# Performance work log

Hardware: AMD Instinct MI355X
Metric: run time of the kernel (lower is better)

Reference implementation:

```python
import jax, jax.numpy as jnp
import numpy as np

B, T, N, F = 8, 24, 207, 16
H = 64            # hidden_dim
DH = 16           # dims_hyper[-1] / node-embedding out
DA = 4 * F        # temporal attention dim_out
DS = 64           # ss_gal gcn out dim (last_ss_gal_dim)
GDEP = 2
ALPHA, BETA, GAMMA = 0.05, 0.95, 0.95
TA = 2.0


def _lin(x, w, b=None):
    y = x @ w
    return y if b is None else y + b


def gcn_hyper(x, A, W, b):
    # x: [B,N,C], A: [N,N] static. h <- a*x + g * einsum('nvc,vw->nwc', h, A)
    h = x
    outs = [h]
    for _ in range(GDEP):
        h = ALPHA * x + GAMMA * jnp.einsum('bvc,vw->bwc', h, A)
        outs.append(h)
    return _lin(jnp.concatenate(outs, axis=-1), W, b)


def gcn_gru(x, A_dyn, A_sta, W, b):
    # x: [B,N,C], A_dyn: [B,N,N], A_sta: [N,N]
    h = x
    outs = [h]
    for _ in range(GDEP):
        h = (ALPHA * x
             + BETA * jnp.einsum('bvw,bvc->bwc', A_dyn, h)     # bmm(A^T, h)
             + GAMMA * jnp.einsum('bvc,vw->bwc', h, A_sta))
        outs.append(h)
    return _lin(jnp.concatenate(outs, axis=-1), W, b)


def gcn_ssgal(x, A, W, b):
    # x: [B*,N,C], A: [B*,N,N]
    h = x
    outs = [h]
    for _ in range(GDEP):
        h = ALPHA * x + GAMMA * jnp.einsum('bvw,bvc->bwc', A, h)
        outs.append(h)
    return _lin(jnp.concatenate(outs, axis=-1), W, b)


def setup_inputs() -> dict:
    key = jax.random.key(0)
    ks = jax.random.split(key, 32)
    i = iter(range(32))
    w = lambda *s: (0.02 * jax.random.normal(ks[next(i)], s, dtype=jnp.float32))
    inp = {
        'input_sequence': jax.random.normal(ks[next(i)], (B, T, N, F), dtype=jnp.float32),
        'static_adj': jax.random.uniform(ks[next(i)], (N, N), dtype=jnp.float32),
        # hyper graph generators: mlp in = (GDEP+1)*H -> DH
        'src_gen_w': w((GDEP + 1) * H, DH), 'src_gen_b': w(DH),
        'tgt_gen_w': w((GDEP + 1) * H, DH), 'tgt_gen_b': w(DH),
        # node embeddings: F -> DH
        'src_emb_w': w(F, DH), 'src_emb_b': w(DH),
        'tgt_emb_w': w(F, DH), 'tgt_emb_b': w(DH),
        # GRU gate GCNs: mlp in = (GDEP+1)*(F+H) -> H
        'gru_z_w': w((GDEP + 1) * (F + H), H), 'gru_z_b': w(H),
        'gru_r_w': w((GDEP + 1) * (F + H), H), 'gru_r_b': w(H),
        'gru_c_w': w((GDEP + 1) * (F + H), H), 'gru_c_b': w(H),
        # temporal attention: F -> DA, score DA -> 1
        'attn_q_w': w(F, DA),
        'attn_k_w': w(F, DA), 'attn_k_b': w(DA),
        'attn_s_w': w(DA, 1),
        # ss_gal spatial gcn: (GDEP+1)*F -> DS
        'sgcn_w': w((GDEP + 1) * F, DS), 'sgcn_b': w(DS),
        # predictors
        'short_w': w(DS, F), 'short_b': w(F),
        'long_w': w(H, F), 'long_b': w(F),
        'fus_w': w(DS + H, F), 'fus_b': w(F),
    }
    return inp


def _forward(input_sequence, static_adj,
             src_gen_w, src_gen_b, tgt_gen_w, tgt_gen_b,
             src_emb_w, src_emb_b, tgt_emb_w, tgt_emb_b,
             gru_z_w, gru_z_b, gru_r_w, gru_r_b, gru_c_w, gru_c_b,
             attn_q_w, attn_k_w, attn_k_b, attn_s_w,
             sgcn_w, sgcn_b,
             short_w, short_b, long_w, long_b, fus_w, fus_b):
    batch, steps, nodes = input_sequence.shape[0], input_sequence.shape[1], input_sequence.shape[2]
    eye = jnp.eye(nodes, dtype=input_sequence.dtype)

    def cell(x_t, h):
        # x_t: [B,N,F], h: [B,N,H]
        src_ctx = gcn_hyper(h, static_adj, src_gen_w, src_gen_b)   # [B,N,DH]
        tgt_ctx = gcn_hyper(h, static_adj, tgt_gen_w, tgt_gen_b)
        s = jnp.tanh(TA * _lin(x_t, src_emb_w, src_emb_b) * src_ctx)
        t = jnp.tanh(TA * _lin(x_t, tgt_emb_w, tgt_emb_b) * tgt_ctx)
        asym = jnp.einsum('bnc,bmc->bnm', s, t) - jnp.einsum('bnc,bmc->bnm', t, s)
        adj = jax.nn.relu(jnp.tanh(TA * asym)) + eye
        adj = adj / (adj.sum(axis=-1, keepdims=True) + 1e-8)
        gi = jnp.concatenate([x_t, h], axis=-1)
        z = jax.nn.sigmoid(gcn_gru(gi, adj, static_adj, gru_z_w, gru_z_b))
        r = jax.nn.sigmoid(gcn_gru(gi, adj, static_adj, gru_r_w, gru_r_b))
        ri = jnp.concatenate([x_t, r * h], axis=-1)
        c = jnp.tanh(gcn_gru(ri, adj, static_adj, gru_c_w, gru_c_b))
        return z * h + (1.0 - z) * c

    h = jnp.zeros((batch, nodes, H), dtype=input_sequence.dtype)
    for t_step in range(0, max(1, steps - 4), 4):
        h = cell(input_sequence[:, t_step], h)

    # ss_gal branch on the last 4 steps
    recent = input_sequence[:, -4:]            # [B,4,N,F]
    target = input_sequence[:, -1]             # [B,N,F]
    # temporal attention
    q = target @ attn_q_w                      # [B,N,DA]
    k = recent @ attn_k_w + attn_k_b           # [B,4,N,DA]
    scores = jnp.tanh(q[:, None, :, None, :] + k[:, :, None, :, :])  # [B,4,N,N,DA]
    scores = jnp.squeeze(scores @ attn_s_w, axis=-1)                  # [B,4,N,N]
    attn = jax.nn.softmax(scores, axis=-1)
    dyn_adj = static_adj[None] + attn.reshape(-1, nodes, nodes)       # [B*4,N,N]
    rh = recent.reshape(-1, nodes, recent.shape[-1])                  # [B*4,N,F]
    rh = gcn_ssgal(rh, dyn_adj, sgcn_w, sgcn_b)                       # [B*4,N,DS]
    rh = jax.nn.relu(rh.reshape(batch, -1, nodes, rh.shape[-1]))      # [B,4,N,DS]
    target = jnp.sum(rh, axis=1)                                       # [B,N,DS]

    short = _lin(target, short_w, short_b)      # [B,N,F]
    h = cell(short, h)                          # final GRU step on short-term prediction
    long = _lin(h, long_w, long_b)              # [B,N,F]
    fused = _lin(jnp.concatenate([target, h], axis=-1), fus_w, fus_b)  # [B,N,F]
    return jnp.stack([short, long, fused], axis=0)  # [3,B,N,F]


def reference(input_sequence, static_adj,
              src_gen_w, src_gen_b, tgt_gen_w, tgt_gen_b,
              src_emb_w, src_emb_b, tgt_emb_w, tgt_emb_b,
              gru_z_w, gru_z_b, gru_r_w, gru_r_b, gru_c_w, gru_c_b,
              attn_q_w, attn_k_w, attn_k_b, attn_s_w,
              sgcn_w, sgcn_b,
              short_w, short_b, long_w, long_b, fus_w, fus_b):
    return _forward(input_sequence, static_adj,
                    src_gen_w, src_gen_b, tgt_gen_w, tgt_gen_b,
                    src_emb_w, src_emb_b, tgt_emb_w, tgt_emb_b,
                    gru_z_w, gru_z_b, gru_r_w, gru_r_b, gru_c_w, gru_c_b,
                    attn_q_w, attn_k_w, attn_k_b, attn_s_w,
                    sgcn_w, sgcn_b,
                    short_w, short_b, long_w, long_b, fus_w, fus_b)
```

## Files before the change

kernel.cpp:

```cpp
#include <hip/hip_runtime.h>


constexpr int B = 8, T = 24, N = 207, F = 16, H = 64, DH = 16;
constexpr int PS = 208;
constexpr float ALPHA = 0.05f, BETA = 0.95f, GAMMA = 0.95f, TA = 2.0f;
constexpr int NF = N * F;
constexpr int BNF = B * N * F;

__device__ __forceinline__ float tanh_fast(float x) { float e = __expf(2.f * x); return 1.f - 2.f / (e + 1.f); }
__device__ __forceinline__ float sigm(float x) { return 1.f / (1.f + __expf(-x)); }
__device__ __forceinline__ float tanh_poly(float x) {
    float x2 = x * x;
    float c = __builtin_fmaf(x2, 0.13333333f, -0.33333333f);
    return x * __builtin_fmaf(x2, c, 1.f);
}

__global__ __launch_bounds__(256) void k_stage0(
    const float* __restrict__ adj, const float* __restrict__ inp,
    const float* __restrict__ Wq, const float* __restrict__ Wk,
    const float* __restrict__ kb, const float* __restrict__ sw_,
    float* __restrict__ Ts, float* __restrict__ A2,
    float* __restrict__ attnT, float* __restrict__ rsum)
{
    __shared__ __align__(16) float smem[7424];
    int bid = blockIdx.x, tid = threadIdx.x;
    if (bid < 49) {
        int vb = (bid % 7) * 32, wb = (bid / 7) * 32;
        float* sA = smem;
        float* sB = smem + 1056;
        float acc[4] = {0, 0, 0, 0};
        int i0 = tid >> 5, j = tid & 31;
        for (int u0 = 0; u0 < N; u0 += 32) {
            __syncthreads();
            for (int l = tid; l < 1024; l += 256) {
                int i = l >> 5, jj = l & 31;
                int v = vb + i, u = u0 + jj;
                sA[i * 33 + jj] = (v < N && u < N) ? adj[v * N + u] : 0.f;
                int uu = u0 + i, w = wb + jj;
                sB[i * 33 + jj] = (uu < N && w < N) ? adj[uu * N + w] : 0.f;
            }
            __syncthreads();
#pragma unroll 8
            for (int u = 0; u < 32; u++) {
                float bv = sB[u * 33 + j];
#pragma unroll
                for (int k = 0; k < 4; k++) acc[k] += sA[(i0 + k * 8) * 33 + u] * bv;
            }
        }
#pragma unroll
        for (int k = 0; k < 4; k++) {
            int v = vb + i0 + k * 8, w = wb + j;
            if (v < N && w < N) A2[(size_t)w * PS + v] = acc[k];
        }
    } else if (bid < 217) {
        int i = (bid - 49) * 256 + tid;
        if (i < N * N) {
            int w = i / N, v = i % N;
            Ts[(size_t)w * PS + v] = adj[v * N + w];
        }
    } else {
        int idx = bid - 217;
        int bt = idx / 49, rem = idx % 49;
        int n0 = (rem % 7) * 32, m0 = (rem / 7) * 32;
        int b = bt >> 2, tau = bt & 3;
        int ti = tid >> 4, tj = tid & 15;
        float* sQ = smem;
        float* sK = smem + 2080;
        float* sWq = smem + 4160;
        float* sWk = smem + 5184;
        float* sXq = smem + 6208;
        float* sXk = smem + 6752;
        float* ssw = smem + 7296;
        float* skb = smem + 7360;
        const float* xq = inp + ((size_t)(b * T + (T - 1))) * NF;
        const float* xk = inp + ((size_t)(b * T + 20 + tau)) * NF;
        {
            float4 wq4 = *(const float4*)&Wq[tid * 4];
            float4 wk4 = *(const float4*)&Wk[tid * 4];
            *(float4*)&sWq[(tid >> 4) * 64 + (tid & 15) * 4] = wq4;
            *(float4*)&sWk[(tid >> 4) * 64 + (tid & 15) * 4] = wk4;
            if (tid < 64) { ssw[tid] = sw_[tid]; skb[tid] = kb[tid]; }
            int i2 = tid & 127;
            int r = i2 >> 2, c4 = (i2 & 3) * 4;
            if (tid < 128) {
                float4 a = make_float4(0, 0, 0, 0);
                int n = n0 + r;
                if (n < N) a = *(const float4*)&xq[(size_t)n * F + c4];
                sXq[r * 17 + c4] = a.x; sXq[r * 17 + c4 + 1] = a.y; sXq[r * 17 + c4 + 2] = a.z; sXq[r * 17 + c4 + 3] = a.w;
            } else {
                float4 c = make_float4(0, 0, 0, 0);
                int m = m0 + r;
                if (m < N) c = *(const float4*)&xk[(size_t)m * F + c4];
                sXk[r * 17 + c4] = c.x; sXk[r * 17 + c4 + 1] = c.y; sXk[r * 17 + c4 + 2] = c.z; sXk[r * 17 + c4 + 3] = c.w;
            }
        }
        __syncthreads();
        {
            int r = tid >> 3, o0 = (tid & 7) * 8;
            float xr[16], xkr[16];
#pragma unroll
            for (int f = 0; f < 16; f++) { xr[f] = sXq[r * 17 + f]; xkr[f] = sXk[r * 17 + f]; }
#pragma unroll
            for (int j = 0; j < 8; j++) {
                int o = o0 + j;
                float aq = 0.f, ak = skb[o];
#pragma unroll
                for (int f = 0; f < 16; f++) { aq += xr[f] * sWq[f * 64 + o]; ak += xkr[f] * sWk[f * 64 + o]; }
                sQ[r * 65 + o] = aq; sK[r * 65 + o] = ak;
            }
        }
        __syncthreads();
        float s00 = 0.f, s01 = 0.f, s10 = 0.f, s11 = 0.f;
#pragma unroll 2
        for (int d = 0; d < 64; d++) {
            float w = ssw[d];
            float q1 = sQ[ti * 65 + d], q2 = sQ[(ti + 16) * 65 + d];
            float k1 = sK[tj * 65 + d], k2 = sK[(tj + 16) * 65 + d];
            s00 += tanh_poly(q1 + k1) * w;
            s01 += tanh_poly(q1 + k2) * w;
            s10 += tanh_poly(q2 + k1) * w;
            s11 += tanh_poly(q2 + k2) * w;
        }
        int n1 = n0 + ti, n2 = n0 + ti + 16, m1 = m0 + tj, m2 = m0 + tj + 16;
        bool vn1 = n1 < N, vn2 = n2 < N, vm1 = m1 < N, vm2 = m2 < N;
        float e00 = (vn1 && vm1) ? __expf(s00) : 0.f;
        float e01 = (vn1 && vm2) ? __expf(s01) : 0.f;
        float e10 = (vn2 && vm1) ? __expf(s10) : 0.f;
        float e11 = (vn2 && vm2) ? __expf(s11) : 0.f;
        float part1 = e00 + e01, part2 = e10 + e11;
        for (int d = 8; d > 0; d >>= 1) {
            part1 += __shfl_down(part1, d, 16);
            part2 += __shfl_down(part2, d, 16);
        }
        if (tj == 0) {
            if (vn1) atomicAdd(&rsum[bt * N + n1], part1);
            if (vn2) atomicAdd(&rsum[bt * N + n2], part2);
        }
        __syncthreads();
        float* tile = sQ;
        tile[tj * 33 + ti] = e00;
        tile[(tj + 16) * 33 + ti] = e01;
        tile[tj * 33 + ti + 16] = e10;
        tile[(tj + 16) * 33 + ti + 16] = e11;
        __syncthreads();
        {
            int row = tid >> 3, c4 = (tid & 7) * 4;
            int m = m0 + row;
            if (m < N) {
                float4 v = make_float4(tile[row * 33 + c4], tile[row * 33 + c4 + 1],
                                       tile[row * 33 + c4 + 2], tile[row * 33 + c4 + 3]);
                *(float4*)&attnT[(size_t)bt * PS * PS + (size_t)m * PS + n0 + c4] = v;
            }
        }
    }
}

__global__ __launch_bounds__(256) void k_cell_a(
    const float* __restrict__ h, const float* __restrict__ Ts, const float* __restrict__ A2,
    const float* __restrict__ xseq, int tsel, const float* __restrict__ xbuf,
    const float* __restrict__ Wsrc, const float* __restrict__ bsrc,
    const float* __restrict__ Wtgt, const float* __restrict__ btgt,
    const float* __restrict__ Wes, const float* __restrict__ bes,
    const float* __restrict__ Wet, const float* __restrict__ bet,
    float* __restrict__ s_out, float* __restrict__ t_out, float* __restrict__ catg) {
    int b = blockIdx.y, w0 = blockIdx.x * 16, lane = blockIdx.z;
    int tid = threadIdx.x, ty = tid >> 4, tx = tid & 15;
    __shared__ float sTs[2][16][33], sA2[2][16][33];
    __shared__ float sH[2][32][64];
    __shared__ float cat[16][193];
    __shared__ float sW[192][16];
    __shared__ float sX[16][16], sWe[16][16];
    float au[4] = {0, 0, 0, 0}, aw[4] = {0, 0, 0, 0};
    const float* hb = h + b * N * H;
    const float* xp = (tsel >= 0) ? (xseq + ((size_t)(b * T + tsel)) * NF) : (xbuf + (size_t)b * NF);
    int pidx = tid & 127;
    int pr = pidx >> 3, pc4 = (pidx & 7) * 4;
    float4 t4;
    float4 h4[2];
    int hr[2], hc[2];
#pragma unroll
    for (int k = 0; k < 2; k++) { int l4 = tid + k * 256; hr[k] = l4 >> 4; hc[k] = (l4 & 15) * 4; }
    auto loadT = [&](int v0) {
        t4 = make_float4(0, 0, 0, 0);
        const float* src = (tid < 128) ? Ts : A2;
        int w = w0 + pr;
        if (w < N) t4 = *(const float4*)&src[(size_t)w * PS + v0 + pc4];
#pragma unroll
        for (int k = 0; k < 2; k++) {
            float4 hv = make_float4(0, 0, 0, 0);
            int v = v0 + hr[k];
            if (v < N) hv = *(const float4*)&hb[(size_t)v * H + hc[k]];
            h4[k] = hv;
        }
    };
    loadT(0);
    int cur = 0;
    for (int t = 0; t < 7; t++) {
        __syncthreads();
        {
            float (*dst)[33] = (tid < 128) ? sTs[cur] : sA2[cur];
            dst[pr][pc4] = t4.x; dst[pr][pc4 + 1] = t4.y; dst[pr][pc4 + 2] = t4.z; dst[pr][pc4 + 3] = t4.w;
        }
#pragma unroll
        for (int k = 0; k < 2; k++) *(float4*)&sH[cur][hr[k]][hc[k]] = h4[k];
        if (t < 6) loadT((t + 1) * 32);
        __syncthreads();
#pragma unroll 8
        for (int v = 0; v < 32; v++) {
            float pu = sTs[cur][ty][v], pw = sA2[cur][ty][v];
#pragma unroll
            for (int j = 0; j < 4; j++) {
                float x = sH[cur][v][tx * 4 + j];
                au[j] += pu * x; aw[j] += pw * x;
            }
        }
        cur ^= 1;
    }
    int w = w0 + ty;
    bool valid = w < N;
    __syncthreads();
    if (valid) {
#pragma unroll
        for (int j = 0; j < 4; j++) {
            int c = tx * 4 + j;
            float hv = hb[(size_t)w * H + c];
            float u = au[j], w2 = aw[j];
            cat[ty][c] = hv;
            cat[ty][64 + c] = ALPHA * hv + GAMMA * u;
            cat[ty][128 + c] = ALPHA * hv + ALPHA * GAMMA * u + GAMMA * GAMMA * w2;
        }
    } else {
#pragma unroll
        for (int j = 0; j < 4; j++) {
            int c = tx * 4 + j;
            cat[ty][c] = 0; cat[ty][64 + c] = 0; cat[ty][128 + c] = 0;
        }
    }
    const float* Wg = lane ? Wtgt : Wsrc;
    const float* bg = lane ? btgt : bsrc;
    const float* We = lane ? Wet : Wes;
    const float* be = lane ? bet : bes;
    {
        float4 wv[3];
#pragma unroll
        for (int k = 0; k < 3; k++) wv[k] = *(const float4*)&Wg[(tid + k * 256) * 4];
        float4 xv = make_float4(0, 0, 0, 0), ev = make_float4(0, 0, 0, 0);
        int sr = 0, sc = 0;
        if (tid < 64) {
            sr = tid >> 2; sc = (tid & 3) * 4;
            int n = w0 + sr;
            if (n < N) xv = *(const float4*)&xp[(size_t)n * F + sc];
            ev = *(const float4*)&We[tid * 4];
        }
#pragma unroll
        for (int k = 0; k < 3; k++) {
            int l4 = tid + k * 256;
            int r = l4 >> 2, c4 = (l4 & 3) * 4;
            *(float4*)&sW[r][c4] = wv[k];
        }
        if (tid < 64) {
            *(float4*)&sX[sr][sc] = xv;
            *(float4*)&sWe[sr][sc] = ev;
        }
    }
    __syncthreads();
    if (lane == 0 && valid) {
#pragma unroll
        for (int j = 0; j < 5; j++) {
            int c = tx * 5 + j;
            float v = (c < 16) ? sX[ty][c] : hb[(size_t)w * H + (c - 16)];
            catg[((size_t)(b * N + w)) * 80 + c] = v;
        }
    }
    {
        float ctx = bg[tx];
#pragma unroll 8
        for (int c = 0; c < 192; c++) ctx += cat[ty][c] * sW[c][tx];
        float xe = be[tx];
#pragma unroll
        for (int f = 0; f < 16; f++) xe += sX[ty][f] * sWe[f][tx];
        if (valid) {
            float val = tanh_fast(TA * xe * ctx);
            if (lane == 0) s_out[(size_t)(b * N + w) * DH + tx] = val;
            else           t_out[(size_t)(b * N + w) * DH + tx] = val;
        }
    }
}

__global__ __launch_bounds__(256) void k_cell_bP(const float* __restrict__ s_in, const float* __restrict__ t_in,
                                                 const float* __restrict__ adj, float* __restrict__ P) {
    int b = blockIdx.y, v0 = blockIdx.x * 16;
    int tid = threadIdx.x, ty = tid >> 4, tx = tid & 15;
    __shared__ float sS[N][17], sT[N][17];
    for (int l4 = tid; l4 < 828; l4 += 256) {
        float4 sv = *(const float4*)&s_in[(size_t)b * N * 16 + l4 * 4];
        float4 tv = *(const float4*)&t_in[(size_t)b * N * 16 + l4 * 4];
        int r = l4 >> 2, c = (l4 & 3) * 4;
        sS[r][c] = sv.x; sS[r][c + 1] = sv.y; sS[r][c + 2] = sv.z; sS[r][c + 3] = sv.w;
        sT[r][c] = tv.x; sT[r][c + 1] = tv.y; sT[r][c + 2] = tv.z; sT[r][c + 3] = tv.w;
    }
    __syncthreads();
    int v = v0 + ty;
    bool valid = v < N;
    int vc = valid ? v : (N - 1);
    float sv[16], tv[16];
#pragma unroll
    for (int k = 0; k < 16; k++) { sv[k] = sS[vc][k]; tv[k] = sT[vc][k]; }
    float val[13];
    float rsum = 0.f;
#pragma unroll
    for (int idx = 0; idx < 13; idx++) {
        int w = tx + 16 * idx;
        float r = 0.f;
        if (w < N) {
            float a = 0.f;
#pragma unroll
            for (int k = 0; k < 16; k++) a += sv[k] * sT[w][k] - tv[k] * sS[w][k];
            r = tanh_fast(TA * a);
            r = r > 0.f ? r : 0.f;
            if (w == v) r += 1.f;
        }
        val[idx] = r;
        rsum += r;
    }
    float tot = rsum;
    for (int d = 8; d > 0; d >>= 1) tot += __shfl_down(tot, d, 16);
    tot = __shfl(tot, 0, 16);
    float rinv = BETA / (tot + 1e-8f);
    if (valid) {
        float* Pb = P + (size_t)b * PS * PS;
#pragma unroll
        for (int idx = 0; idx < 13; idx++) {
            int w = tx + 16 * idx;
            if (w < N) Pb[(size_t)w * PS + v] = val[idx] * rinv + GAMMA * adj[v * N + w];
        }
    }
}

__device__ __forceinline__ void body_prop_xr(float* smem, int w0, int bt,
    const float* __restrict__ attnT, const float* __restrict__ rsum,
    const float* __restrict__ Ts, const float* __restrict__ inp, float* __restrict__ x1)
{
    int b = bt >> 2, tau = bt & 3;
    const float* xb = inp + ((size_t)(b * T + 20 + tau)) * NF;
    const float* PA = attnT + (size_t)bt * PS * PS;
    int tid = threadIdx.x, ty = tid >> 4, tx = tid & 15;
    float (*sPA)[16][33] = (float(*)[16][33])(smem);
    float (*sPT)[16][33] = (float(*)[16][33])(smem + 1056);
    float (*sX)[32][17]  = (float(*)[32][17])(smem + 2112);
    float (*sXs)[32][17] = (float(*)[32][17])(smem + 3200);
    float accA = 0.f, accT = 0.f;
    int prr = tid >> 3, pcc = (tid & 7) * 4;
    int xrr = (tid - 128) >> 2, xcc = ((tid - 128) & 3) * 4;
    float4 pa, pt, xv;
    float rinv_;
    auto loadT = [&](int v0) {
        pa = make_float4(0, 0, 0, 0); pt = make_float4(0, 0, 0, 0); xv = make_float4(0, 0, 0, 0); rinv_ = 0.f;
        if (tid < 128) {
            int w = w0 + prr;
            if (w < N) {
                pa = *(const float4*)&PA[(size_t)w * PS + v0 + pcc];
                pt = *(const float4*)&Ts[(size_t)w * PS + v0 + pcc];
            }
        } else {
            int v = v0 + xrr;
            if (v < N) {
                xv = *(const float4*)&xb[(size_t)v * F + xcc];
                rinv_ = __builtin_amdgcn_rcpf(rsum[bt * N + v]);
            }
        }
    };
    loadT(0);
    int cur = 0;
    for (int t = 0; t < 7; t++) {
        __syncthreads();
        if (tid < 128) {
            sPA[cur][prr][pcc] = pa.x; sPA[cur][prr][pcc + 1] = pa.y; sPA[cur][prr][pcc + 2] = pa.z; sPA[cur][prr][pcc + 3] = pa.w;
            sPT[cur][prr][pcc] = pt.x; sPT[cur][prr][pcc + 1] = pt.y; sPT[cur][prr][pcc + 2] = pt.z; sPT[cur][prr][pcc + 3] = pt.w;
        } else {
            sX[cur][xrr][xcc] = xv.x; sX[cur][xrr][xcc + 1] = xv.y; sX[cur][xrr][xcc + 2] = xv.z; sX[cur][xrr][xcc + 3] = xv.w;
            sXs[cur][xrr][xcc] = xv.x * rinv_; sXs[cur][xrr][xcc + 1] = xv.y * rinv_;
            sXs[cur][xrr][xcc + 2] = xv.z * rinv_; sXs[cur][xrr][xcc + 3] = xv.w * rinv_;
        }
        if (t < 6) loadT((t + 1) * 32);
        __syncthreads();
#pragma unroll 8
        for (int v = 0; v < 32; v++) {
            accA += sPA[cur][ty][v] * sXs[cur][v][tx];
            accT += sPT[cur][ty][v] * sX[cur][v][tx];
        }
        cur ^= 1;
    }
    int w = w0 + ty;
    if (w < N) x1[((size_t)(bt * N + w)) * 16 + tx] = ALPHA * xb[w * F + tx] + GAMMA * (accA + accT);
}

__device__ __forceinline__ void body_sgc2(float* smem, int w0, int bt,
    const float* __restrict__ attnT, const float* __restrict__ rsum,
    const float* __restrict__ Ts, const float* __restrict__ x1, const float* __restrict__ inp,
    const float* __restrict__ Ws, const float* __restrict__ bs, float* __restrict__ target)
{
    int b = bt >> 2, tau = bt & 3;
    const float* xb = inp + ((size_t)(b * T + 20 + tau)) * NF;
    const float* PA = attnT + (size_t)bt * PS * PS;
    int tid = threadIdx.x, ty = tid >> 4, tx = tid & 15;
    float (*sPA)[16][33] = (float(*)[16][33])(smem);
    float (*sPT)[16][33] = (float(*)[16][33])(smem + 1056);
    float (*sX)[32][17]  = (float(*)[32][17])(smem + 2112);
    float (*sXs)[32][17] = (float(*)[32][17])(smem + 3200);
    float (*scat)[48]    = (float(*)[48])(smem + 4288);
    float (*sWs)[64]     = (float(*)[64])(smem + 5056);
    float accA = 0.f, accT = 0.f;
    int prr = tid >> 3, pcc = (tid & 7) * 4;
    int xrr = (tid - 128) >> 2, xcc = ((tid - 128) & 3) * 4;
    float4 pa, pt, xv;
    float rinv_;
    auto loadT = [&](int v0) {
        pa = make_float4(0, 0, 0, 0); pt = make_float4(0, 0, 0, 0); xv = make_float4(0, 0, 0, 0); rinv_ = 0.f;
        if (tid < 128) {
            int w = w0 + prr;
            if (w < N) {
                pa = *(const float4*)&PA[(size_t)w * PS + v0 + pcc];
                pt = *(const float4*)&Ts[(size_t)w * PS + v0 + pcc];
            }
        } else {
            int v = v0 + xrr;
            if (v < N) {
                xv = *(const float4*)&x1[((size_t)(bt * N + v)) * 16 + xcc];
                rinv_ = __builtin_amdgcn_rcpf(rsum[bt * N + v]);
            }
        }
    };
    loadT(0);
    int cur = 0;
    for (int t = 0; t < 7; t++) {
        __syncthreads();
        if (tid < 128) {
            sPA[cur][prr][pcc] = pa.x; sPA[cur][prr][pcc + 1] = pa.y; sPA[cur][prr][pcc + 2] = pa.z; sPA[cur][prr][pcc + 3] = pa.w;
            sPT[cur][prr][pcc] = pt.x; sPT[cur][prr][pcc + 1] = pt.y; sPT[cur][prr][pcc + 2] = pt.z; sPT[cur][prr][pcc + 3] = pt.w;
        } else {
            sX[cur][xrr][xcc] = xv.x; sX[cur][xrr][xcc + 1] = xv.y; sX[cur][xrr][xcc + 2] = xv.z; sX[cur][xrr][xcc + 3] = xv.w;
            sXs[cur][xrr][xcc] = xv.x * rinv_; sXs[cur][xrr][xcc + 1] = xv.y * rinv_;
            sXs[cur][xrr][xcc + 2] = xv.z * rinv_; sXs[cur][xrr][xcc + 3] = xv.w * rinv_;
        }
        if (t < 6) loadT((t + 1) * 32);
        __syncthreads();
#pragma unroll 8
        for (int v = 0; v < 32; v++) {
            accA += sPA[cur][ty][v] * sXs[cur][v][tx];
            accT += sPT[cur][ty][v] * sX[cur][v][tx];
        }
        cur ^= 1;
    }
    int w = w0 + ty;
    bool valid = w < N;
    __syncthreads();
    for (int l = tid; l < 512; l += 256) {
        int i = l >> 5, c = l & 31;
        int ww = w0 + i;
        float vv = 0;
        if (ww < N) {
            if (c < 16) vv = xb[ww * F + c];
            else vv = x1[((size_t)bt * N + ww) * 16 + (c - 16)];
        }
        scat[i][c] = vv;
    }
    {
        float x0 = valid ? xb[w * F + tx] : 0.f;
        scat[ty][32 + tx] = ALPHA * x0 + GAMMA * (accA + accT);
    }
    {
        float4 wv[3];
#pragma unroll
        for (int k = 0; k < 3; k++) wv[k] = *(const float4*)&Ws[(tid + k * 256) * 4];
#pragma unroll
        for (int k = 0; k < 3; k++) {
            int l4 = tid + k * 256;
            *(float4*)&sWs[l4 >> 4][(l4 & 15) * 4] = wv[k];
        }
    }
    __syncthreads();
    float a[4];
#pragma unroll
    for (int j = 0; j < 4; j++) a[j] = bs[tx * 4 + j];
#pragma unroll 8
    for (int cc = 0; cc < 48; cc++) {
        float cv = scat[ty][cc];
        float4 w4 = *(const float4*)&sWs[cc][tx * 4];
        a[0] += cv * w4.x; a[1] += cv * w4.y; a[2] += cv * w4.z; a[3] += cv * w4.w;
    }
    if (valid) {
#pragma unroll
        for (int j = 0; j < 4; j++) {
            float r = a[j] > 0.f ? a[j] : 0.f;
            atomicAdd(&target[(b * N + w) * 64 + tx * 4 + j], r);
        }
    }
}

__device__ __forceinline__ void body_short(float* smem, int n0, int b,
    const float* __restrict__ target, const float* __restrict__ Wsh, const float* __restrict__ bsh,
    float* __restrict__ out, float* __restrict__ xshort)
{
    int tid = threadIdx.x, ty = tid >> 4, tx = tid & 15;
    float (*trow)[65] = (float(*)[65])(smem);
    float (*sW)[16]   = (float(*)[16])(smem + 1040);
    {
        int r = tid >> 4, c4 = (tid & 15) * 4;
        int n = n0 + r;
        float4 tv = make_float4(0, 0, 0, 0);
        if (n < N) tv = *(const float4*)&target[((size_t)(b * N + n)) * 64 + c4];
        trow[r][c4] = tv.x; trow[r][c4 + 1] = tv.y; trow[r][c4 + 2] = tv.z; trow[r][c4 + 3] = tv.w;
        float4 wv = *(const float4*)&Wsh[tid * 4];
        *(float4*)&sW[tid >> 2][(tid & 3) * 4] = wv;
    }
    __syncthreads();
    float a = bsh[tx];
#pragma unroll 8
    for (int o = 0; o < 64; o++) a += trow[ty][o] * sW[o][tx];
    int n = n0 + ty;
    if (n < N) {
        out[((size_t)0 * B * N + b * N + n) * 16 + tx] = a;
        xshort[(b * N + n) * 16 + tx] = a;
    }
}

__global__ __launch_bounds__(256) void k_psq(
    const float* __restrict__ P, float* __restrict__ P2, int aux,
    const float* __restrict__ attnT, const float* __restrict__ rsum,
    const float* __restrict__ Ts, const float* __restrict__ inp, float* __restrict__ x1,
    const float* __restrict__ Ws, const float* __restrict__ bs, float* __restrict__ target,
    const float* __restrict__ Wsh, const float* __restrict__ bsh,
    float* __restrict__ out, float* __restrict__ xshort)
{
    __shared__ __align__(16) float smem[8128];
    int bid = blockIdx.x, tid = threadIdx.x;
    if (bid < 1352) {
        int b = bid / 169, r = bid % 169;
        int w0 = (r % 13) * 16, v0 = (r / 13) * 16;
        const float* Pb = P + (size_t)b * PS * PS;
        float (*sA)[16][33] = (float(*)[16][33])(smem);
        float (*sB)[32][17] = (float(*)[32][17])(smem + 1056);
        int ty = tid >> 4, tx = tid & 15;
        int ar = tid >> 4, ac = (tid & 15) * 2;
        int br = tid >> 3, bc = (tid & 7) * 2;
        float2 av, bv;
        auto loadT = [&](int u0) {
            av = make_float2(0, 0); bv = make_float2(0, 0);
            int w = w0 + ar;
            if (w < N) av = *(const float2*)&Pb[(size_t)w * PS + u0 + ac];
            int u = u0 + br;
            if (u < N) bv = *(const float2*)&Pb[(size_t)u * PS + v0 + bc];
        };
        loadT(0);
        int cur = 0;
        float acc = 0.f;
        for (int t = 0; t < 7; t++) {
            __syncthreads();
            sA[cur][ar][ac] = av.x; sA[cur][ar][ac + 1] = av.y;
            sB[cur][br][bc] = bv.x; sB[cur][br][bc + 1] = bv.y;
            if (t < 6) loadT((t + 1) * 32);
            __syncthreads();
#pragma unroll 8
            for (int u = 0; u < 32; u++) acc += sA[cur][ty][u] * sB[cur][u][tx];
            cur ^= 1;
        }
        int w = w0 + ty, v = v0 + tx;
        if (w < N && v < N) P2[(size_t)b * PS * PS + (size_t)w * PS + v] = acc;
    } else {
        int idx = bid - 1352;
        if (aux == 1)      body_prop_xr(smem, (idx % 13) * 16, idx / 13, attnT, rsum, Ts, inp, x1);
        else if (aux == 2) body_sgc2(smem, (idx % 13) * 16, idx / 13, attnT, rsum, Ts, x1, inp, Ws, bs, target);
        else               body_short(smem, (idx % 13) * 16, idx / 13, target, Wsh, bsh, out, xshort);
    }
}

__global__ __launch_bounds__(256) void k_gate2(
    const float* __restrict__ cat, const float* __restrict__ P, const float* __restrict__ P2,
    const float* __restrict__ Wa, const float* __restrict__ ba,
    const float* __restrict__ Wb, const float* __restrict__ bb,
    int baseMode,
    const float* __restrict__ xseq, int tsel, const float* __restrict__ xbuf,
    float* __restrict__ zbuf, float* __restrict__ ricat,
    float* __restrict__ h,
    const float* __restrict__ target,
    const float* __restrict__ Wlong, const float* __restrict__ blong,
    const float* __restrict__ Wfus, const float* __restrict__ bfus,
    float* __restrict__ out) {
    int mode = baseMode + blockIdx.z;
    const float* W = (mode == 1) ? Wb : Wa;
    const float* bias = (mode == 1) ? bb : ba;
    int b = blockIdx.y, w0 = blockIdx.x * 16;
    int tid = threadIdx.x, ty = tid >> 4, tx = tid & 15;
    const float* Pb = P + (size_t)b * PS * PS;
    const float* Qb = P2 + (size_t)b * PS * PS;
    __shared__ float sC[16][241];
    __shared__ float sP[16][33], sQ[16][33];
    __shared__ float sX[32][81];
    __shared__ float sW[48][65];
    __shared__ float hrow[16][65], trow[16][65];
    for (int l4 = tid; l4 < 320; l4 += 256) {
        int r = l4 / 20, c4 = (l4 % 20) * 4;
        int w = w0 + r;
        float4 v4 = make_float4(0, 0, 0, 0);
        if (w < N) v4 = *(const float4*)&cat[((size_t)(b * N + w)) * 80 + c4];
        sC[r][c4] = v4.x; sC[r][c4 + 1] = v4.y; sC[r][c4 + 2] = v4.z; sC[r][c4 + 3] = v4.w;
    }
    float accP[5] = {0, 0, 0, 0, 0}, accQ[5] = {0, 0, 0, 0, 0};
    int prr = tid >> 4, prc = (tid & 15) * 2;
    int xrow = tid & 31, xc0 = (tid >> 5) * 10;
    float2 pv, qv;
    float2 xv[5];
    auto loadT = [&](int v0) {
        pv = make_float2(0, 0); qv = make_float2(0, 0);
        int w = w0 + prr;
        if (w < N) {
            pv = *(const float2*)&Pb[(size_t)w * PS + v0 + prc];
            qv = *(const float2*)&Qb[(size_t)w * PS + v0 + prc];
        }
        int v = v0 + xrow;
#pragma unroll
        for (int k = 0; k < 5; k++) xv[k] = make_float2(0, 0);
        if (v < N) {
            const float* src = &cat[((size_t)(b * N + v)) * 80 + xc0];
#pragma unroll
            for (int k = 0; k < 5; k++) xv[k] = *(const float2*)&src[k * 2];
        }
    };
    loadT(0);
    for (int t = 0; t < 7; t++) {
        __syncthreads();
        sP[prr][prc] = pv.x; sP[prr][prc + 1] = pv.y;
        sQ[prr][prc] = qv.x; sQ[prr][prc + 1] = qv.y;
#pragma unroll
        for (int k = 0; k < 5; k++) { sX[xrow][xc0 + 2 * k] = xv[k].x; sX[xrow][xc0 + 2 * k + 1] = xv[k].y; }
        if (t < 6) loadT((t + 1) * 32);
        __syncthreads();
#pragma unroll 8
        for (int v = 0; v < 32; v++) {
            float p = sP[ty][v], q = sQ[ty][v];
#pragma unroll
            for (int j = 0; j < 5; j++) {
                float x = sX[v][tx * 5 + j];
                accP[j] += p * x;
                accQ[j] += q * x;
            }
        }
    }
#pragma unroll
    for (int j = 0; j < 5; j++) {
        int c = tx * 5 + j;
        float g0 = sC[ty][c];
        sC[ty][80 + c]  = ALPHA * g0 + accP[j];
        sC[ty][160 + c] = ALPHA * g0 + ALPHA * accP[j] + accQ[j];
    }
    float4 wv[3];
#pragma unroll
    for (int k = 0; k < 3; k++) wv[k] = *(const float4*)&W[(tid + k * 256) * 4];
    float ga[4];
#pragma unroll
    for (int j = 0; j < 4; j++) ga[j] = bias[tx * 4 + j];
    for (int ch = 0; ch < 5; ch++) {
        __syncthreads();
#pragma unroll
        for (int k = 0; k < 3; k++) {
            int l4 = tid + k * 256;
            int r = l4 >> 4, cc = (l4 & 15) * 4;
            sW[r][cc] = wv[k].x; sW[r][cc + 1] = wv[k].y; sW[r][cc + 2] = wv[k].z; sW[r][cc + 3] = wv[k].w;
        }
        if (ch < 4) {
#pragma unroll
            for (int k = 0; k < 3; k++) wv[k] = *(const float4*)&W[(size_t)(ch + 1) * 3072 + (tid + k * 256) * 4];
        }
        __syncthreads();
        int c0 = ch * 48;
#pragma unroll 8
        for (int cc = 0; cc < 48; cc++) {
            float cv = sC[ty][c0 + cc];
#pragma unroll
            for (int j = 0; j < 4; j++) ga[j] += cv * sW[cc][tx * 4 + j];
        }
    }
    int w = w0 + ty;
    bool valid = w < N;
    if (mode == 0) {
        if (valid) {
#pragma unroll
            for (int j = 0; j < 4; j++) zbuf[((size_t)(b * N + w)) * 64 + tx * 4 + j] = sigm(ga[j]);
        }
    } else if (mode == 1) {
        if (valid) {
#pragma unroll
            for (int j = 0; j < 4; j++) {
                int o = tx * 4 + j;
                ricat[((size_t)(b * N + w)) * 80 + 16 + o] = sigm(ga[j]) * h[((size_t)(b * N + w)) * 64 + o];
            }
            if (tx < 4) {
                const float* xp = (tsel >= 0) ? (xseq + ((size_t)(b * T + tsel)) * NF) : (xbuf + (size_t)b * NF);
#pragma unroll
                for (int j = 0; j < 4; j++) {
                    int c = tx * 4 + j;
                    ricat[((size_t)(b * N + w)) * 80 + c] = xp[w * F + c];
                }
            }
        }
    } else {
#pragma unroll
        for (int j = 0; j < 4; j++) {
            int o = tx * 4 + j;
            float cval = tanh_fast(ga[j]);
            float zv = 0.f, hv = 0.f;
            if (valid) { zv = zbuf[((size_t)(b * N + w)) * 64 + o]; hv = h[((size_t)(b * N + w)) * 64 + o]; }
            float hn = zv * hv + (1.f - zv) * cval;
            if (valid) h[((size_t)(b * N + w)) * 64 + o] = hn;
            hrow[ty][o] = valid ? hn : 0.f;
        }
        if (mode == 3) {
            for (int l = tid; l < 1024; l += 256) {
                int i = l >> 6, o = l & 63;
                int ww = w0 + i;
                trow[i][o] = (ww < N) ? target[((size_t)(b * N + ww)) * 64 + o] : 0.f;
            }
            __syncthreads();
            float lg = blong[tx];
            float fs = bfus[tx];
#pragma unroll 8
            for (int o = 0; o < 64; o++) {
                lg += hrow[ty][o] * Wlong[o * 16 + tx];
                fs += trow[ty][o] * Wfus[o * 16 + tx] + hrow[ty][o] * Wfus[(64 + o) * 16 + tx];
            }
            if (valid) {
                out[((size_t)1 * B * N + b * N + w) * 16 + tx] = lg;
                out[((size_t)2 * B * N + b * N + w) * 16 + tx] = fs;
            }
        }
    }
}

extern "C" void kernel_launch(void* const* d_in, const int* in_sizes, int n_in,
                              void* d_out, int out_size, void* d_ws, size_t ws_size,
                              hipStream_t stream) {
    const float* inp = (const float*)d_in[0];
    const float* adj = (const float*)d_in[1];
    const float* src_gen_w = (const float*)d_in[2];
    const float* src_gen_b = (const float*)d_in[3];
    const float* tgt_gen_w = (const float*)d_in[4];
    const float* tgt_gen_b = (const float*)d_in[5];
    const float* src_emb_w = (const float*)d_in[6];
    const float* src_emb_b = (const float*)d_in[7];
    const float* tgt_emb_w = (const float*)d_in[8];
    const float* tgt_emb_b = (const float*)d_in[9];
    const float* gru_z_w = (const float*)d_in[10];
    const float* gru_z_b = (const float*)d_in[11];
    const float* gru_r_w = (const float*)d_in[12];
    const float* gru_r_b = (const float*)d_in[13];
    const float* gru_c_w = (const float*)d_in[14];
    const float* gru_c_b = (const float*)d_in[15];
    const float* attn_q_w = (const float*)d_in[16];
    const float* attn_k_w = (const float*)d_in[17];
    const float* attn_k_b = (const float*)d_in[18];
    const float* attn_s_w = (const float*)d_in[19];
    const float* sgcn_w = (const float*)d_in[20];
    const float* sgcn_b = (const float*)d_in[21];
    const float* short_w = (const float*)d_in[22];
    const float* short_b = (const float*)d_in[23];
    const float* long_w = (const float*)d_in[24];
    const float* long_b = (const float*)d_in[25];
    const float* fus_w = (const float*)d_in[26];
    const float* fus_b = (const float*)d_in[27];
    float* out = (float*)d_out;

    float* ws = (float*)d_ws;
    size_t off = 0;
    auto A = [&](size_t n) { n = (n + 3) & ~(size_t)3; float* p = ws + off; off += n; return p; };
    float* Ts = A((size_t)PS * PS);
    float* A2 = A((size_t)PS * PS);
    float* sbuf = A((size_t)B * N * DH);
    float* tbuf = A((size_t)B * N * DH);
    float* P = A((size_t)B * PS * PS);
    float* P2 = A((size_t)B * PS * PS);
    float* catg = A((size_t)B * N * 80);
    float* catc = A((size_t)B * N * 80);
    float* zb = A((size_t)B * N * 64);
    float* attnT = A((size_t)32 * PS * PS);
    float* x1 = A((size_t)32 * NF);
    float* xshort = A(BNF);
    size_t zero_begin = off;
    float* h = A((size_t)B * N * H);
    float* target = A((size_t)B * N * 64);
    float* rsum = A((size_t)32 * N);
    size_t zero_end = off;
    (void)ws_size; (void)in_sizes; (void)n_in; (void)out_size;

    hipMemsetAsync(h, 0, (zero_end - zero_begin) * sizeof(float), stream);
    k_stage0<<<1785, 256, 0, stream>>>(adj, inp, attn_q_w, attn_k_w, attn_k_b, attn_s_w, Ts, A2, attnT, rsum);

    auto run_cell = [&](int tsel, const float* xbuf, int finalFlag, int aux) {
        k_cell_a<<<dim3(13, B, 2), 256, 0, stream>>>(h, Ts, A2, inp, tsel, xbuf,
                                                     src_gen_w, src_gen_b, tgt_gen_w, tgt_gen_b,
                                                     src_emb_w, src_emb_b, tgt_emb_w, tgt_emb_b, sbuf, tbuf, catg);
        k_cell_bP<<<dim3(13, B), 256, 0, stream>>>(sbuf, tbuf, adj, P);
        int extra = (aux == 1 || aux == 2) ? 416 : (aux == 3 ? 104 : 0);
        k_psq<<<1352 + extra, 256, 0, stream>>>(P, P2, aux, attnT, rsum, Ts, inp, x1,
                                                sgcn_w, sgcn_b, target, short_w, short_b, out, xshort);
        k_gate2<<<dim3(13, B, 2), 256, 0, stream>>>(catg, P, P2, gru_z_w, gru_z_b, gru_r_w, gru_r_b, 0,
                                                    inp, tsel, xbuf, zb, catc, h,
                                                    nullptr, nullptr, nullptr, nullptr, nullptr, nullptr);
        k_gate2<<<dim3(13, B, 1), 256, 0, stream>>>(catc, P, P2, gru_c_w, gru_c_b, nullptr, nullptr, 2 + finalFlag,
                                                    nullptr, 0, nullptr, zb, nullptr, h,
                                                    target, long_w, long_b, fus_w, fus_b, out);
    };

    run_cell(0, nullptr, 0, 1);
    run_cell(4, nullptr, 0, 2);
    run_cell(8, nullptr, 0, 3);
    run_cell(12, nullptr, 0, 0);
    run_cell(16, nullptr, 0, 0);

    run_cell(-1, xshort, 1, 0);
}
```

Before: 629.9 us.

## Fold first-step hyper-graph cell into stage0 and retile adjacency kernel

Because h is zero at the first step, the hyper-graph context reduces to the generator biases. The first k_cell_a work (node embeddings, s/t outputs and the catg input slice) is now computed by extra blocks appended to k_stage0, and the first k_cell_a launch is skipped. This removes one launch and the redundant GCN-over-zero work. Separately, k_cell_bP is retiled to 8 rows by 32 columns per block with twice as many blocks, which raises parallelism. The risk is that the zero-h shortcut depends on the memset ordering and on catg columns being zeroed correctly.

```diff
diff --git a/kernel.cpp b/kernel.cpp
--- a/kernel.cpp
+++ b/kernel.cpp
@@ -19,8 +19,12 @@
     const float* __restrict__ adj, const float* __restrict__ inp,
     const float* __restrict__ Wq, const float* __restrict__ Wk,
     const float* __restrict__ kb, const float* __restrict__ sw_,
+    const float* __restrict__ Wes, const float* __restrict__ bes,
+    const float* __restrict__ Wet, const float* __restrict__ bet,
+    const float* __restrict__ bsrc, const float* __restrict__ btgt,
     float* __restrict__ Ts, float* __restrict__ A2,
-    float* __restrict__ attnT, float* __restrict__ rsum)
+    float* __restrict__ attnT, float* __restrict__ rsum,
+    float* __restrict__ s_out, float* __restrict__ t_out, float* __restrict__ catg)
 {
     __shared__ __align__(16) float smem[7424];
     int bid = blockIdx.x, tid = threadIdx.x;
@@ -58,7 +62,7 @@
             int w = i / N, v = i % N;
             Ts[(size_t)w * PS + v] = adj[v * N + w];
         }
-    } else {
+    } else if (bid < 1785) {
         int idx = bid - 217;
         int bt = idx / 49, rem = idx % 49;
         int n0 = (rem % 7) * 32, m0 = (rem / 7) * 32;
@@ -83,15 +87,15 @@
             int i2 = tid & 127;
             int r = i2 >> 2, c4 = (i2 & 3) * 4;
             if (tid < 128) {
-                float4 a = make_float4(0, 0, 0, 0);
+                float4 aq = make_float4(0, 0, 0, 0);
                 int n = n0 + r;
-                if (n < N) a = *(const float4*)&xq[(size_t)n * F + c4];
-                sXq[r * 17 + c4] = a.x; sXq[r * 17 + c4 + 1] = a.y; sXq[r * 17 + c4 + 2] = a.z; sXq[r * 17 + c4 + 3] = a.w;
+                if (n < N) aq = *(const float4*)&xq[(size_t)n * F + c4];
+                sXq[r * 17 + c4] = aq.x; sXq[r * 17 + c4 + 1] = aq.y; sXq[r * 17 + c4 + 2] = aq.z; sXq[r * 17 + c4 + 3] = aq.w;
             } else {
-                float4 c = make_float4(0, 0, 0, 0);
+                float4 ck = make_float4(0, 0, 0, 0);
                 int m = m0 + r;
-                if (m < N) c = *(const float4*)&xk[(size_t)m * F + c4];
-                sXk[r * 17 + c4] = c.x; sXk[r * 17 + c4 + 1] = c.y; sXk[r * 17 + c4 + 2] = c.z; sXk[r * 17 + c4 + 3] = c.w;
+                if (m < N) ck = *(const float4*)&xk[(size_t)m * F + c4];
+                sXk[r * 17 + c4] = ck.x; sXk[r * 17 + c4 + 1] = ck.y; sXk[r * 17 + c4 + 2] = ck.z; sXk[r * 17 + c4 + 3] = ck.w;
             }
         }
         __syncthreads();
@@ -151,6 +155,37 @@
                                        tile[row * 33 + c4 + 2], tile[row * 33 + c4 + 3]);
                 *(float4*)&attnT[(size_t)bt * PS * PS + (size_t)m * PS + n0 + c4] = v;
             }
+        }
+    } else {
+        int idx = bid - 1785;
+        int x13 = idx % 13, b = idx / 13;
+        int w0 = x13 * 16;
+        int ty = tid >> 4, tx = tid & 15;
+        float* sX  = smem;
+        float* sWs = smem + 272;
+        float* sWt = smem + 528;
+        const float* xp = inp + ((size_t)(b * T + 0)) * NF;
+        {
+            int w = w0 + ty;
+            sX[ty * 17 + tx] = (w < N) ? xp[(size_t)w * F + tx] : 0.f;
+            sWs[ty * 16 + tx] = Wes[ty * 16 + tx];
+            sWt[ty * 16 + tx] = Wet[ty * 16 + tx];
+        }
+        __syncthreads();
+        float xs = bes[tx], xt = bet[tx];
+#pragma unroll
+        for (int f = 0; f < 16; f++) {
+            float xv = sX[ty * 17 + f];
+            xs += xv * sWs[f * 16 + tx];
+            xt += xv * sWt[f * 16 + tx];
+        }
+        int w = w0 + ty;
+        if (w < N) {
+            s_out[((size_t)(b * N + w)) * DH + tx] = tanh_fast(TA * xs * bsrc[tx]);
+            t_out[((size_t)(b * N + w)) * DH + tx] = tanh_fast(TA * xt * btgt[tx]);
+            catg[((size_t)(b * N + w)) * 80 + tx] = sX[ty * 17 + tx];
+#pragma unroll
+            for (int j = 0; j < 4; j++) catg[((size_t)(b * N + w)) * 80 + 16 + tx * 4 + j] = 0.f;
         }
     }
 }
@@ -289,8 +324,8 @@
 
 __global__ __launch_bounds__(256) void k_cell_bP(const float* __restrict__ s_in, const float* __restrict__ t_in,
                                                  const float* __restrict__ adj, float* __restrict__ P) {
-    int b = blockIdx.y, v0 = blockIdx.x * 16;
-    int tid = threadIdx.x, ty = tid >> 4, tx = tid & 15;
+    int b = blockIdx.y, v0 = blockIdx.x * 8;
+    int tid = threadIdx.x, ty = tid >> 5, tx = tid & 31;
     __shared__ float sS[N][17], sT[N][17];
     for (int l4 = tid; l4 < 828; l4 += 256) {
         float4 sv = *(const float4*)&s_in[(size_t)b * N * 16 + l4 * 4];
@@ -306,11 +341,11 @@
     float sv[16], tv[16];
 #pragma unroll
     for (int k = 0; k < 16; k++) { sv[k] = sS[vc][k]; tv[k] = sT[vc][k]; }
-    float val[13];
+    float val[7];
     float rsum = 0.f;
 #pragma unroll
-    for (int idx = 0; idx < 13; idx++) {
-        int w = tx + 16 * idx;
+    for (int idx = 0; idx < 7; idx++) {
+        int w = tx + 32 * idx;
         float r = 0.f;
         if (w < N) {
             float a = 0.f;
@@ -324,14 +359,14 @@
         rsum += r;
     }
     float tot = rsum;
-    for (int d = 8; d > 0; d >>= 1) tot += __shfl_down(tot, d, 16);
-    tot = __shfl(tot, 0, 16);
+    for (int d = 16; d > 0; d >>= 1) tot += __shfl_down(tot, d, 32);
+    tot = __shfl(tot, 0, 32);
     float rinv = BETA / (tot + 1e-8f);
     if (valid) {
         float* Pb = P + (size_t)b * PS * PS;
 #pragma unroll
-        for (int idx = 0; idx < 13; idx++) {
-            int w = tx + 16 * idx;
+        for (int idx = 0; idx < 7; idx++) {
+            int w = tx + 32 * idx;
             if (w < N) Pb[(size_t)w * PS + v] = val[idx] * rinv + GAMMA * adj[v * N + w];
         }
     }
@@ -480,19 +515,19 @@
         }
     }
     __syncthreads();
-    float a[4];
-#pragma unroll
-    for (int j = 0; j < 4; j++) a[j] = bs[tx * 4 + j];
+    float acc[4];
+#pragma unroll
+    for (int j = 0; j < 4; j++) acc[j] = bs[tx * 4 + j];
 #pragma unroll 8
     for (int cc = 0; cc < 48; cc++) {
         float cv = scat[ty][cc];
         float4 w4 = *(const float4*)&sWs[cc][tx * 4];
-        a[0] += cv * w4.x; a[1] += cv * w4.y; a[2] += cv * w4.z; a[3] += cv * w4.w;
+        acc[0] += cv * w4.x; acc[1] += cv * w4.y; acc[2] += cv * w4.z; acc[3] += cv * w4.w;
     }
     if (valid) {
 #pragma unroll
         for (int j = 0; j < 4; j++) {
-            float r = a[j] > 0.f ? a[j] : 0.f;
+            float r = acc[j] > 0.f ? acc[j] : 0.f;
             atomicAdd(&target[(b * N + w) * 64 + tx * 4 + j], r);
         }
     }
@@ -515,13 +550,13 @@
         *(float4*)&sW[tid >> 2][(tid & 3) * 4] = wv;
     }
     __syncthreads();
-    float a = bsh[tx];
-#pragma unroll 8
-    for (int o = 0; o < 64; o++) a += trow[ty][o] * sW[o][tx];
+    float acc = bsh[tx];
+#pragma unroll 8
+    for (int o = 0; o < 64; o++) acc += trow[ty][o] * sW[o][tx];
     int n = n0 + ty;
     if (n < N) {
-        out[((size_t)0 * B * N + b * N + n) * 16 + tx] = a;
-        xshort[(b * N + n) * 16 + tx] = a;
+        out[((size_t)0 * B * N + b * N + n) * 16 + tx] = acc;
+        xshort[(b * N + n) * 16 + tx] = acc;
     }
 }
 
@@ -793,13 +828,17 @@
     (void)ws_size; (void)in_sizes; (void)n_in; (void)out_size;
 
     hipMemsetAsync(h, 0, (zero_end - zero_begin) * sizeof(float), stream);
-    k_stage0<<<1785, 256, 0, stream>>>(adj, inp, attn_q_w, attn_k_w, attn_k_b, attn_s_w, Ts, A2, attnT, rsum);
-
-    auto run_cell = [&](int tsel, const float* xbuf, int finalFlag, int aux) {
-        k_cell_a<<<dim3(13, B, 2), 256, 0, stream>>>(h, Ts, A2, inp, tsel, xbuf,
-                                                     src_gen_w, src_gen_b, tgt_gen_w, tgt_gen_b,
-                                                     src_emb_w, src_emb_b, tgt_emb_w, tgt_emb_b, sbuf, tbuf, catg);
-        k_cell_bP<<<dim3(13, B), 256, 0, stream>>>(sbuf, tbuf, adj, P);
+    k_stage0<<<1889, 256, 0, stream>>>(adj, inp, attn_q_w, attn_k_w, attn_k_b, attn_s_w,
+                                       src_emb_w, src_emb_b, tgt_emb_w, tgt_emb_b,
+                                       src_gen_b, tgt_gen_b,
+                                       Ts, A2, attnT, rsum, sbuf, tbuf, catg);
+
+    auto run_cell = [&](int tsel, const float* xbuf, int finalFlag, int aux, bool skipA) {
+        if (!skipA)
+            k_cell_a<<<dim3(13, B, 2), 256, 0, stream>>>(h, Ts, A2, inp, tsel, xbuf,
+                                                         src_gen_w, src_gen_b, tgt_gen_w, tgt_gen_b,
+                                                         src_emb_w, src_emb_b, tgt_emb_w, tgt_emb_b, sbuf, tbuf, catg);
+        k_cell_bP<<<dim3(26, B), 256, 0, stream>>>(sbuf, tbuf, adj, P);
         int extra = (aux == 1 || aux == 2) ? 416 : (aux == 3 ? 104 : 0);
         k_psq<<<1352 + extra, 256, 0, stream>>>(P, P2, aux, attnT, rsum, Ts, inp, x1,
                                                 sgcn_w, sgcn_b, target, short_w, short_b, out, xshort);
@@ -811,11 +850,11 @@
                                                     target, long_w, long_b, fus_w, fus_b, out);
     };
 
-    run_cell(0, nullptr, 0, 1);
-    run_cell(4, nullptr, 0, 2);
-    run_cell(8, nullptr, 0, 3);
-    run_cell(12, nullptr, 0, 0);
-    run_cell(16, nullptr, 0, 0);
-
-    run_cell(-1, xshort, 1, 0);
-}
+    run_cell(0, nullptr, 0, 1, true);
+    run_cell(4, nullptr, 0, 2, false);
+    run_cell(8, nullptr, 0, 3, false);
+    run_cell(12, nullptr, 0, 0, false);
+    run_cell(16, nullptr, 0, 0, false);
+
+    run_cell(-1, xshort, 1, 0, false);
+}
```

Measured after the change: 606.5 us. -3.7%, faster.
